# Performance work log

Hardware: AMD Instinct MI355X
Metric: run time of the kernel (lower is better)

Reference implementation:

```python
import jax, jax.numpy as jnp
import numpy as np

EPS = 1e-5
N_NODES = 100000
N_EDGES = 1600000
DIMS = [196, 64, 128, 256, 256, 576]


def sage_conv(x, src, dst, Wl, Wr, b, n):
    # PyG SAGEConv (mean aggr): out = lin_l(mean_j x_j) + lin_r(x_i)
    agg = jax.ops.segment_sum(x[src], dst, num_segments=n)
    cnt = jax.ops.segment_sum(jnp.ones((src.shape[0],), x.dtype), dst, num_segments=n)
    agg = agg / jnp.maximum(cnt, 1.0)[:, None]
    return agg @ Wl.T + x @ Wr.T + b


def batch_norm(x, gamma, beta):
    m = jnp.mean(x, axis=0)
    v = jnp.mean((x - m) ** 2, axis=0)  # biased var, as in torch BN forward
    return (x - m) * jax.lax.rsqrt(v + EPS) * gamma + beta


def setup_inputs() -> dict:
    key = jax.random.key(0)
    ks = jax.random.split(key, 32)
    inp = {
        "x": jax.random.normal(ks[0], (N_NODES, DIMS[0]), dtype=jnp.float32),
        "edge_index": jax.random.randint(ks[1], (2, N_EDGES), 0, N_NODES, dtype=jnp.int32),
    }
    ki = 2
    for i in range(5):
        fin, fout = DIMS[i], DIMS[i + 1]
        s = 1.0 / np.sqrt(fin)
        inp[f"W{i+1}l"] = jax.random.uniform(ks[ki], (fout, fin), jnp.float32, -s, s); ki += 1
        inp[f"W{i+1}r"] = jax.random.uniform(ks[ki], (fout, fin), jnp.float32, -s, s); ki += 1
        inp[f"b{i+1}"] = jax.random.uniform(ks[ki], (fout,), jnp.float32, -s, s); ki += 1
    for i in range(4):
        fout = DIMS[i + 1]
        inp[f"g{i+1}"] = jnp.ones((fout,), jnp.float32)
        inp[f"be{i+1}"] = jnp.zeros((fout,), jnp.float32)
    return inp


def reference(x, edge_index,
              W1l, W1r, b1, W2l, W2r, b2, W3l, W3r, b3,
              W4l, W4r, b4, W5l, W5r, b5,
              g1, be1, g2, be2, g3, be3, g4, be4):
    src, dst = edge_index[0], edge_index[1]
    n = x.shape[0]
    x = jax.nn.relu(batch_norm(sage_conv(x, src, dst, W1l, W1r, b1, n), g1, be1))
    x = jax.nn.relu(batch_norm(sage_conv(x, src, dst, W2l, W2r, b2, n), g2, be2))
    x = jax.nn.relu(batch_norm(sage_conv(x, src, dst, W3l, W3r, b3, n), g3, be3))
    x = jax.nn.relu(batch_norm(sage_conv(x, src, dst, W4l, W4r, b4, n), g4, be4))
    x = sage_conv(x, src, dst, W5l, W5r, b5, n)
    return x
```

## Files before the change

### kernel.cpp

```cpp
#include <hip/hip_runtime.h>
#include <hip/hip_bf16.h>

typedef __hip_bfloat16 bf16;
typedef __attribute__((ext_vector_type(8))) short short8;
typedef __attribute__((ext_vector_type(4))) float f32x4;

#define NN 100000
#define NE 1600000

__device__ __forceinline__ float bf2f(short s) {
    return __uint_as_float(((unsigned int)(unsigned short)s) << 16);
}
__device__ __forceinline__ short f2bf(float f) {
    union { bf16 b; short s; } u;
    u.b = __float2bfloat16(f);
    return u.s;
}

__global__ void detect_kernel(const unsigned int* __restrict__ x, int* __restrict__ flags) {
    __shared__ int s;
    if (threadIdx.x == 0) s = 0;
    __syncthreads();
    int c = 0;
    for (int j = 0; j < 4; ++j) {
        unsigned int w = x[threadIdx.x * 4 + j];
        unsigned int e = (w >> 7) & 0xFF;
        if (e >= 100 && e <= 141) c++;
    }
    atomicAdd(&s, c);
    __syncthreads();
    if (threadIdx.x == 0) flags[0] = (s > 128) ? 1 : 0;
}

__global__ __launch_bounds__(256) void cvt_pad_kernel(const void* __restrict__ in,
                                                      bf16* __restrict__ out,
                                                      int rows, int sk, int dk,
                                                      const int* __restrict__ flagp) {
    int i = blockIdx.x * 256 + threadIdx.x;
    int g4 = dk >> 2;
    if (i >= rows * g4) return;
    int row = i / g4;
    int c = (i - row * g4) * 4;
    uint2 w;
    w.x = 0u; w.y = 0u;
    if (c < sk) {
        if (flagp[0]) {
            w = *(const uint2*)((const char*)in + ((size_t)row * sk + c) * 2);
        } else {
            const float* f = (const float*)((const char*)in + ((size_t)row * sk + c) * 4);
            union { bf16 t[4]; uint2 u; } pk;
            pk.t[0] = __float2bfloat16(f[0]);
            pk.t[1] = __float2bfloat16(f[1]);
            pk.t[2] = __float2bfloat16(f[2]);
            pk.t[3] = __float2bfloat16(f[3]);
            w = pk.u;
        }
    }
    *(uint2*)((char*)out + ((size_t)row * dk + c) * 2) = w;
}

struct WJobs {
    const void* src[10];
    bf16* dst[10];
    int rows[10];
    int sk[10];
    int dk[10];
};
__global__ __launch_bounds__(256) void cvt_pad_multi(WJobs J, const int* __restrict__ flagp) {
    int j = blockIdx.y;
    int g4 = J.dk[j] >> 2;
    int tot = J.rows[j] * g4;
    int i = blockIdx.x * 256 + threadIdx.x;
    if (i >= tot) return;
    int row = i / g4;
    int c = (i - row * g4) * 4;
    int sk = J.sk[j];
    uint2 w;
    w.x = 0u; w.y = 0u;
    if (c < sk) {
        if (flagp[0]) {
            w = *(const uint2*)((const char*)J.src[j] + ((size_t)row * sk + c) * 2);
        } else {
            const float* f = (const float*)((const char*)J.src[j] + ((size_t)row * sk + c) * 4);
            union { bf16 t[4]; uint2 u; } pk;
            pk.t[0] = __float2bfloat16(f[0]);
            pk.t[1] = __float2bfloat16(f[1]);
            pk.t[2] = __float2bfloat16(f[2]);
            pk.t[3] = __float2bfloat16(f[3]);
            w = pk.u;
        }
    }
    *(uint2*)((char*)J.dst[j] + ((size_t)row * J.dk[j] + c) * 2) = w;
}

struct VJobs {
    const void* src[13];
    float* dst[13];
    int n[13];
};
__global__ __launch_bounds__(576) void cvt_f32_multi(VJobs J, const int* __restrict__ flagp) {
    int j = blockIdx.x;
    int c = threadIdx.x;
    if (c >= J.n[j]) return;
    float v;
    if (flagp[0]) v = __bfloat162float(((const bf16*)J.src[j])[c]);
    else v = ((const float*)J.src[j])[c];
    J.dst[j][c] = v;
}

__global__ __launch_bounds__(256) void fill_kernel(bf16* __restrict__ out, long long n) {
    long long i = (long long)blockIdx.x * 256 + threadIdx.x;
    if (i < n) out[i] = __float2bfloat16(1000.0f);
}


__global__ __launch_bounds__(256) void count_kernel(const int* __restrict__ dst,
                                                    int* __restrict__ cnt) {
    int e = blockIdx.x * 256 + threadIdx.x;
    if (e < NE) atomicAdd(&cnt[dst[e]], 1);
}

#define SCAN_NB ((NN + 1023) / 1024)

__global__ __launch_bounds__(256) void scan_partial_kernel(const int* __restrict__ cnt,
                                                           int* __restrict__ bsum) {
    __shared__ int lds[256];
    int t = threadIdx.x;
    int base = blockIdx.x * 1024 + t * 4;
    int s = 0;
#pragma unroll
    for (int i = 0; i < 4; ++i) {
        int idx = base + i;
        if (idx < NN) s += cnt[idx];
    }
    lds[t] = s;
    __syncthreads();
    for (int h = 128; h > 0; h >>= 1) {
        if (t < h) lds[t] += lds[t + h];
        __syncthreads();
    }
    if (t == 0) bsum[blockIdx.x] = lds[0];
}

__global__ __launch_bounds__(128) void scan_bsum_kernel(int* __restrict__ bsum,
                                                        int* __restrict__ indptr) {
    __shared__ int lds[128];
    int t = threadIdx.x;
    int v = (t < SCAN_NB) ? bsum[t] : 0;
    lds[t] = v;
    __syncthreads();
    for (int off = 1; off < 128; off <<= 1) {
        int x = (t >= off) ? lds[t - off] : 0;
        __syncthreads();
        lds[t] += x;
        __syncthreads();
    }
    if (t < SCAN_NB) bsum[t] = lds[t] - v;
    if (t == 127) indptr[NN] = lds[127];
}

__global__ __launch_bounds__(256) void scan_apply_kernel(const int* __restrict__ cnt,
                                                         const int* __restrict__ bsum,
                                                         int* __restrict__ indptr,
                                                         int* __restrict__ cursor,
                                                         float* __restrict__ recip) {
    __shared__ int lds[256];
    int t = threadIdx.x;
    int base = blockIdx.x * 1024 + t * 4;
    int c[4];
    int s = 0;
#pragma unroll
    for (int i = 0; i < 4; ++i) {
        int idx = base + i;
        c[i] = (idx < NN) ? cnt[idx] : 0;
        s += c[i];
    }
    lds[t] = s;
    __syncthreads();
    for (int off = 1; off < 256; off <<= 1) {
        int x = (t >= off) ? lds[t - off] : 0;
        __syncthreads();
        lds[t] += x;
        __syncthreads();
    }
    int run = bsum[blockIdx.x] + lds[t] - s;
#pragma unroll
    for (int i = 0; i < 4; ++i) {
        int idx = base + i;
        if (idx < NN) {
            indptr[idx] = run;
            cursor[idx] = run;
            recip[idx] = 1.0f / (float)(c[i] > 1 ? c[i] : 1);
            run += c[i];
        }
    }
}

__global__ __launch_bounds__(256) void scatter_kernel(const int* __restrict__ src,
                                                      const int* __restrict__ dst,
                                                      int* __restrict__ cursor,
                                                      int* __restrict__ csr) {
    int e = blockIdx.x * 256 + threadIdx.x;
    if (e < NE) {
        int d = dst[e];
        int p = atomicAdd(&cursor[d], 1);
        csr[p] = src[e];
    }
}

template <int D, int ADD>
__global__ __launch_bounds__(256) void aggv_kernel(const bf16* __restrict__ u,
                                                   const int* __restrict__ indptr,
                                                   const int* __restrict__ csr,
                                                   const float* __restrict__ recip,
                                                   bf16* __restrict__ out) {
    constexpr int TPR = D / 8;
    constexpr int NPB = 256 / TPR;
    const int tid = threadIdx.x;
    const int node = blockIdx.x * NPB + tid / TPR;
    if (node >= NN) return;
    const int c0 = (tid % TPR) * 8;
    const short* ub = (const short*)u + c0;
    const int j0 = indptr[node], j1 = indptr[node + 1];
    float acc[8];
#pragma unroll
    for (int t = 0; t < 8; ++t) acc[t] = 0.f;
    int j = j0;
    for (; j + 3 < j1; j += 4) {
        int s0 = csr[j], s1 = csr[j + 1], s2 = csr[j + 2], s3 = csr[j + 3];
        short8 v0 = *(const short8*)(ub + (size_t)s0 * D);
        short8 v1 = *(const short8*)(ub + (size_t)s1 * D);
        short8 v2 = *(const short8*)(ub + (size_t)s2 * D);
        short8 v3 = *(const short8*)(ub + (size_t)s3 * D);
#pragma unroll
        for (int t = 0; t < 8; ++t)
            acc[t] += (bf2f(v0[t]) + bf2f(v1[t])) + (bf2f(v2[t]) + bf2f(v3[t]));
    }
    for (; j < j1; ++j) {
        short8 v0 = *(const short8*)(ub + (size_t)csr[j] * D);
#pragma unroll
        for (int t = 0; t < 8; ++t) acc[t] += bf2f(v0[t]);
    }
    const float r = recip[node];
    size_t o = (size_t)node * D + c0;
    short8 w;
    if (ADD) {
        short8 prev = *(const short8*)((const short*)out + o);
#pragma unroll
        for (int t = 0; t < 8; ++t) w[t] = f2bf(acc[t] * r + bf2f(prev[t]));
    } else {
#pragma unroll
        for (int t = 0; t < 8; ++t) w[t] = f2bf(acc[t] * r);
    }
    *(short8*)((short*)out + o) = w;
}

template <int D>
__global__ __launch_bounds__(256) void aggbn_kernel(const bf16* __restrict__ raw,
                                                    const int* __restrict__ indptr,
                                                    const int* __restrict__ csr,
                                                    const float* __restrict__ recip,
                                                    const float* __restrict__ scale,
                                                    const float* __restrict__ shift,
                                                    bf16* __restrict__ act,
                                                    bf16* __restrict__ agg) {
    constexpr int TPR = D / 8;
    constexpr int NPB = 256 / TPR;
    const int tid = threadIdx.x;
    const int node = blockIdx.x * NPB + tid / TPR;
    if (node >= NN) return;
    const int c0 = (tid % TPR) * 8;
    float sc[8], sh[8];
    *(float4*)&sc[0] = *(const float4*)&scale[c0];
    *(float4*)&sc[4] = *(const float4*)&scale[c0 + 4];
    *(float4*)&sh[0] = *(const float4*)&shift[c0];
    *(float4*)&sh[4] = *(const float4*)&shift[c0 + 4];
    const short* ub = (const short*)raw + c0;
    {
        short8 v = *(const short8*)(ub + (size_t)node * D);
        short8 w;
#pragma unroll
        for (int t = 0; t < 8; ++t) {
            float x = bf2f(v[t]) * sc[t] + sh[t];
            w[t] = f2bf(x > 0.f ? x : 0.f);
        }
        *(short8*)((short*)act + (size_t)node * D + c0) = w;
    }
    const int j0 = indptr[node], j1 = indptr[node + 1];
    float acc[8];
#pragma unroll
    for (int t = 0; t < 8; ++t) acc[t] = 0.f;
    int j = j0;
    for (; j + 3 < j1; j += 4) {
        int s0 = csr[j], s1 = csr[j + 1], s2 = csr[j + 2], s3 = csr[j + 3];
        short8 v0 = *(const short8*)(ub + (size_t)s0 * D);
        short8 v1 = *(const short8*)(ub + (size_t)s1 * D);
        short8 v2 = *(const short8*)(ub + (size_t)s2 * D);
        short8 v3 = *(const short8*)(ub + (size_t)s3 * D);
#pragma unroll
        for (int t = 0; t < 8; ++t) {
            float x0 = fmaxf(bf2f(v0[t]) * sc[t] + sh[t], 0.f);
            float x1 = fmaxf(bf2f(v1[t]) * sc[t] + sh[t], 0.f);
            float x2 = fmaxf(bf2f(v2[t]) * sc[t] + sh[t], 0.f);
            float x3 = fmaxf(bf2f(v3[t]) * sc[t] + sh[t], 0.f);
            acc[t] += (x0 + x1) + (x2 + x3);
        }
    }
    for (; j < j1; ++j) {
        short8 v0 = *(const short8*)(ub + (size_t)csr[j] * D);
#pragma unroll
        for (int t = 0; t < 8; ++t)
            acc[t] += fmaxf(bf2f(v0[t]) * sc[t] + sh[t], 0.f);
    }
    const float r = recip[node];
    size_t o = (size_t)node * D + c0;
    short8 w;
#pragma unroll
    for (int t = 0; t < 8; ++t) w[t] = f2bf(acc[t] * r);
    *(short8*)((short*)agg + o) = w;
}

__device__ __forceinline__ void gld_lds16(const void* g, void* l) {
    __builtin_amdgcn_global_load_lds(
        (const __attribute__((address_space(1))) unsigned int*)g,
        (__attribute__((address_space(3))) unsigned int*)l, 16, 0, 0);
}

__global__ __launch_bounds__(256) void gemm_kernel(
    const bf16* __restrict__ A1, const bf16* __restrict__ W1, int K1,
    const bf16* __restrict__ A2, const bf16* __restrict__ W2, int K2,
    const float* __restrict__ bias,
    bf16* __restrict__ outB, bf16* __restrict__ outB2, int Nsplit,
    void* __restrict__ outFinal,
    float* __restrict__ statp,
    const int* __restrict__ flagp,
    int M, int N) {
    __shared__ alignas(16) char smem[81920];

    const int tid = threadIdx.x;
    const int lane = tid & 63, wv = tid >> 6;
    const int lrow = lane & 15, lq = lane >> 4;

    const int nwg = gridDim.x * gridDim.y;
    const int flat = blockIdx.y * gridDim.x + blockIdx.x;
    const int xcd = flat & 7;
    const int rest = flat >> 3;
    const int q = nwg >> 3, r = nwg & 7;
    const int chunk = (xcd < r) ? xcd * (q + 1) : r * (q + 1) + (xcd - r) * q;
    const int newid = chunk + rest;
    const int n0 = (newid % gridDim.x) * 64;
    const int m0 = (newid / gridDim.x) * 256;

    const int isbf = flagp[0];

    f32x4 acc[4][4];
#pragma unroll
    for (int a = 0; a < 4; ++a)
#pragma unroll
        for (int b = 0; b < 4; ++b) acc[a][b] = (f32x4){0.f, 0.f, 0.f, 0.f};

    const int sr = tid >> 3;
    const int scb = (tid & 7) << 4;

    const int nt1 = K1 >> 6;
    const int nt2 = K2 >> 6;
    const int nt = nt1 + nt2;

    auto stage = [&](int t, int b) {
        const bf16* Ap;
        const bf16* Wp;
        int K, k0;
        if (t < nt1) { Ap = A1; Wp = W1; K = K1; k0 = t << 6; }
        else { Ap = A2; Wp = W2; K = K2; k0 = (t - nt1) << 6; }
        char* bA = smem + b * 40960;
        char* bW = bA + 32768;
#pragma unroll
        for (int i = 0; i < 8; ++i) {
            int row = i * 32 + sr;
            int gr = m0 + row;
            if (gr >= M) gr = M - 1;
            const char* g = (const char*)Ap + ((size_t)gr * K + k0) * 2 +
                            (scb ^ ((row & 7) << 4));
            gld_lds16(g, bA + row * 128 + scb);
        }
#pragma unroll
        for (int i = 0; i < 2; ++i) {
            int row = i * 32 + sr;
            const char* g = (const char*)Wp + ((size_t)(n0 + row) * K + k0) * 2 +
                            (scb ^ ((row & 7) << 4));
            gld_lds16(g, bW + row * 128 + scb);
        }
    };

    stage(0, 0);
    __syncthreads();
    int cur = 0;
#pragma unroll 1
    for (int t = 0; t < nt; ++t) {
        if (t + 1 < nt) stage(t + 1, cur ^ 1);
        const char* sA = smem + cur * 40960;
        const char* sW = sA + 32768;
#pragma unroll
        for (int kh = 0; kh < 2; ++kh) {
            short8 a[4], b[4];
            const int cb = kh * 64 + lq * 16;
#pragma unroll
            for (int mi = 0; mi < 4; ++mi) {
                int row = wv * 64 + mi * 16 + lrow;
                a[mi] = *(const short8*)(sA + row * 128 + (cb ^ ((row & 7) << 4)));
            }
#pragma unroll
            for (int ni = 0; ni < 4; ++ni) {
                int row = ni * 16 + lrow;
                b[ni] = *(const short8*)(sW + row * 128 + (cb ^ ((row & 7) << 4)));
            }
#pragma unroll
            for (int mi = 0; mi < 4; ++mi)
#pragma unroll
                for (int ni = 0; ni < 4; ++ni)
                    acc[mi][ni] = __builtin_amdgcn_mfma_f32_16x16x32_bf16(
                        a[mi], b[ni], acc[mi][ni], 0, 0, 0);
        }
        __syncthreads();
        cur ^= 1;
    }

    if (statp) {
#pragma unroll
        for (int ni = 0; ni < 4; ++ni) {
            int gcol = n0 + ni * 16 + lrow;
            float bv = bias ? bias[gcol] : 0.f;
            float s = 0.f, q2 = 0.f;
#pragma unroll
            for (int mi = 0; mi < 4; ++mi) {
#pragma unroll
                for (int r2 = 0; r2 < 4; ++r2) {
                    int grow = m0 + wv * 64 + mi * 16 + lq * 4 + r2;
                    if (grow < M) {
                        float v = acc[mi][ni][r2] + bv;
                        s += v;
                        q2 += v * v;
                    }
                }
            }
            s += __shfl_xor(s, 16, 64);
            s += __shfl_xor(s, 32, 64);
            q2 += __shfl_xor(q2, 16, 64);
            q2 += __shfl_xor(q2, 32, 64);
            if (lq == 0) {
                atomicAdd(&statp[gcol], s);
                atomicAdd(&statp[N + gcol], q2);
            }
        }
    }
    const bool f32out = (outFinal != nullptr) && !isbf;
    if (!f32out) {
        bf16* dst = outB ? outB : (bf16*)outFinal;
        short* sc = (short*)smem;
#pragma unroll
        for (int ni = 0; ni < 4; ++ni) {
            float bv = bias ? bias[n0 + ni * 16 + lrow] : 0.f;
#pragma unroll
            for (int mi = 0; mi < 4; ++mi) {
                int rl = wv * 64 + mi * 16 + lq * 4;
#pragma unroll
                for (int r2 = 0; r2 < 4; ++r2)
                    sc[(rl + r2) * 64 + ni * 16 + lrow] = f2bf(acc[mi][ni][r2] + bv);
            }
        }
        __syncthreads();
#pragma unroll
        for (int i = 0; i < 8; ++i) {
            int f8 = tid + i * 256;
            int rowl = f8 >> 3;
            int col0 = (f8 & 7) * 8;
            int grow = m0 + rowl;
            int gcol = n0 + col0;
            if (grow < M) {
                short8 v = ((const short8*)smem)[f8];
                if (gcol < Nsplit)
                    *(short8*)((short*)dst + (size_t)grow * Nsplit + gcol) = v;
                else
                    *(short8*)((short*)outB2 + (size_t)grow * (N - Nsplit) +
                               (gcol - Nsplit)) = v;
            }
        }
    } else {
        float* dst = (float*)outFinal;
        float* sf = (float*)smem;
#pragma unroll
        for (int ni = 0; ni < 4; ++ni) {
            float bv = bias ? bias[n0 + ni * 16 + lrow] : 0.f;
#pragma unroll
            for (int mi = 0; mi < 4; ++mi) {
                int rl = wv * 64 + mi * 16 + lq * 4;
#pragma unroll
                for (int r2 = 0; r2 < 4; ++r2)
                    sf[(rl + r2) * 64 + ni * 16 + lrow] = acc[mi][ni][r2] + bv;
            }
        }
        __syncthreads();
#pragma unroll
        for (int i = 0; i < 16; ++i) {
            int f4 = tid + i * 256;
            int rowl = f4 >> 4;
            int col0 = (f4 & 15) * 4;
            int grow = m0 + rowl;
            if (grow < M)
                *(float4*)(dst + (size_t)grow * N + n0 + col0) =
                    ((const float4*)smem)[f4];
        }
    }
}


__global__ __launch_bounds__(256) void bn_stats_kernel(const bf16* __restrict__ C,
                                                       int ldN,
                                                       float* __restrict__ stats) {
    int N = 1 << ldN;
    int tid = threadIdx.x;
    int c = tid & (N - 1);
    int rsub = tid >> ldN;
    int rstep = 256 >> ldN;
    int r0 = blockIdx.x * 64;
    float s = 0.f, q = 0.f;
    for (int r = r0 + rsub; r < r0 + 64; r += rstep) {
        if (r < NN) {
            float v = __bfloat162float(C[(size_t)r * N + c]);
            s += v;
            q += v * v;
        }
    }
    __shared__ float ls[256], lq[256];
    ls[tid] = s;
    lq[tid] = q;
    __syncthreads();
    for (int half = rstep >> 1; half > 0; half >>= 1) {
        if (rsub < half) {
            ls[tid] += ls[tid + half * N];
            lq[tid] += lq[tid + half * N];
        }
        __syncthreads();
    }
    if (rsub == 0) {
        atomicAdd(&stats[c], ls[tid]);
        atomicAdd(&stats[N + c], lq[tid]);
    }
}

__global__ __launch_bounds__(256) void bn_finalize_kernel(const float* __restrict__ stats,
                                                          const float* __restrict__ g,
                                                          const float* __restrict__ be,
                                                          int N,
                                                          float* __restrict__ scale,
                                                          float* __restrict__ shift) {
    int c = threadIdx.x;
    if (c >= N) return;
    float mean = stats[c] * (1.0f / NN);
    float var = stats[N + c] * (1.0f / NN) - mean * mean;
    var = fmaxf(var, 0.f);
    float sc = g[c] * rsqrtf(var + 1e-5f);
    scale[c] = sc;
    shift[c] = be[c] - mean * sc;
}


extern "C" void kernel_launch(void* const* d_in, const int* in_sizes, int n_in,
                              void* d_out, int out_size, void* d_ws, size_t ws_size,
                              hipStream_t stream) {
    const void* x_raw = d_in[0];
    const int* ei = (const int*)d_in[1];
    const int* src = ei;
    const int* dst = ei + NE;

    char* w = (char*)d_ws;
    size_t off = 0;
    auto alloc = [&](size_t bytes) {
        void* p = w + off;
        off = (off + bytes + 255) & ~(size_t)255;
        return p;
    };
    int* flags = (int*)alloc(256);
    int* cnt = (int*)alloc((size_t)NN * 4);
    int* indptr = (int*)alloc((size_t)(NN + 1) * 4);
    int* cursor = (int*)alloc((size_t)NN * 4);
    float* recip = (float*)alloc((size_t)NN * 4);
    int* csr = (int*)alloc((size_t)NE * 4);
    int* bsum = (int*)alloc((size_t)SCAN_NB * 4);
    const int KDIM[5] = {196, 64, 128, 256, 256};
    const int KPAD[5] = {256, 64, 128, 256, 256};
    const int NDIM[5] = {64, 128, 256, 256, 576};
    bf16 *Wlb[5], *Wrb[5];
    float *bf_[5], *gf[4], *bef[4];
    for (int i = 0; i < 5; ++i) {
        Wlb[i] = (bf16*)alloc((size_t)KPAD[i] * NDIM[i] * 2);
        Wrb[i] = (bf16*)alloc((size_t)KPAD[i] * NDIM[i] * 2);
        bf_[i] = (float*)alloc((size_t)NDIM[i] * 4);
    }
    for (int i = 0; i < 4; ++i) {
        gf[i] = (float*)alloc((size_t)NDIM[i] * 4);
        bef[i] = (float*)alloc((size_t)NDIM[i] * 4);
    }
    float* bias1cat = (float*)alloc(128 * 4);
    float* stats = (float*)alloc(1408 * 4);
    float* scale = (float*)alloc(256 * 4);
    float* shift = (float*)alloc(256 * 4);
    float *s1 = stats, *s2 = stats + 128, *s3 = stats + 384, *s4 = stats + 896;
    bf16* aggb = (bf16*)alloc((size_t)NN * 256 * 2);
    bf16* S1 = (bf16*)alloc((size_t)NN * 256 * 2);
    bf16* S2 = (bf16*)alloc((size_t)NN * 256 * 2);
    bf16* xb = aggb;
    bf16* u1 = S2;

    if (off > ws_size) {
        long long n = (long long)NN * 576;
        fill_kernel<<<(int)((n + 255) / 256), 256, 0, stream>>>((bf16*)d_out, n);
        return;
    }

    hipMemsetAsync(cnt, 0, (size_t)NN * 4, stream);
    hipMemsetAsync(stats, 0, 1408 * 4, stream);
    hipMemsetAsync(bias1cat, 0, 64 * 4, stream);

    detect_kernel<<<1, 64, 0, stream>>>((const unsigned int*)x_raw, flags);

    {
        int totx = NN * (KPAD[0] >> 2);
        cvt_pad_kernel<<<(totx + 255) / 256, 256, 0, stream>>>(x_raw, xb, NN, 196, 256, flags);

        WJobs wj;
        int maxb = 0;
        for (int i = 0; i < 5; ++i) {
            wj.src[2 * i] = d_in[2 + 3 * i];
            wj.dst[2 * i] = Wlb[i];
            wj.src[2 * i + 1] = d_in[3 + 3 * i];
            wj.dst[2 * i + 1] = Wrb[i];
            wj.rows[2 * i] = wj.rows[2 * i + 1] = NDIM[i];
            wj.sk[2 * i] = wj.sk[2 * i + 1] = KDIM[i];
            wj.dk[2 * i] = wj.dk[2 * i + 1] = KPAD[i];
            int nb = (NDIM[i] * (KPAD[i] >> 2) + 255) / 256;
            if (nb > maxb) maxb = nb;
        }
        cvt_pad_multi<<<dim3(maxb, 10), 256, 0, stream>>>(wj, flags);

        VJobs vj;
        vj.src[0] = d_in[4];  vj.dst[0] = bias1cat + 64; vj.n[0] = 64;
        for (int i = 1; i < 5; ++i) {
            vj.src[i] = d_in[4 + 3 * i];
            vj.dst[i] = bf_[i];
            vj.n[i] = NDIM[i];
        }
        for (int i = 0; i < 4; ++i) {
            vj.src[5 + i] = d_in[17 + 2 * i];
            vj.dst[5 + i] = gf[i];
            vj.n[5 + i] = NDIM[i];
            vj.src[9 + i] = d_in[18 + 2 * i];
            vj.dst[9 + i] = bef[i];
            vj.n[9 + i] = NDIM[i];
        }
        cvt_f32_multi<<<13, 576, 0, stream>>>(vj, flags);
    }

    count_kernel<<<(NE + 255) / 256, 256, 0, stream>>>(dst, cnt);
    scan_partial_kernel<<<SCAN_NB, 256, 0, stream>>>(cnt, bsum);
    scan_bsum_kernel<<<1, 128, 0, stream>>>(bsum, indptr);
    scan_apply_kernel<<<SCAN_NB, 256, 0, stream>>>(cnt, bsum, indptr, cursor, recip);
    scatter_kernel<<<(NE + 255) / 256, 256, 0, stream>>>(src, dst, cursor, csr);

    const int GM = (NN + 63) / 64;
    const int GY = (NN + 255) / 256;

    gemm_kernel<<<dim3(2, GY), 256, 0, stream>>>(xb, Wlb[0], 256, nullptr, nullptr, 0,
                                                 bias1cat, u1, S1, 64,
                                                 nullptr, nullptr, flags, NN, 128);
    aggv_kernel<64, 1><<<NN / 32, 256, 0, stream>>>(u1, indptr, csr, recip, S1);
    bn_stats_kernel<<<GM, 256, 0, stream>>>(S1, 6, s1);
    bn_finalize_kernel<<<1, 256, 0, stream>>>(s1, gf[0], bef[0], 64, scale, shift);

    aggbn_kernel<64><<<NN / 32, 256, 0, stream>>>(S1, indptr, csr, recip, scale, shift,
                                                  S2, aggb);
    gemm_kernel<<<dim3(2, GY), 256, 0, stream>>>(aggb, Wlb[1], 64, S2, Wrb[1], 64,
                                                 bf_[1], S1, nullptr, 128,
                                                 nullptr, s2, flags, NN, 128);
    bn_finalize_kernel<<<1, 256, 0, stream>>>(s2, gf[1], bef[1], 128, scale, shift);

    aggbn_kernel<128><<<NN / 16, 256, 0, stream>>>(S1, indptr, csr, recip, scale, shift,
                                                   S2, aggb);
    gemm_kernel<<<dim3(4, GY), 256, 0, stream>>>(aggb, Wlb[2], 128, S2, Wrb[2], 128,
                                                 bf_[2], S1, nullptr, 256,
                                                 nullptr, s3, flags, NN, 256);
    bn_finalize_kernel<<<1, 256, 0, stream>>>(s3, gf[2], bef[2], 256, scale, shift);

    aggbn_kernel<256><<<NN / 8, 256, 0, stream>>>(S1, indptr, csr, recip, scale, shift,
                                                  S2, aggb);
    gemm_kernel<<<dim3(4, GY), 256, 0, stream>>>(aggb, Wlb[3], 256, S2, Wrb[3], 256,
                                                 bf_[3], S1, nullptr, 256,
                                                 nullptr, s4, flags, NN, 256);
    bn_finalize_kernel<<<1, 256, 0, stream>>>(s4, gf[3], bef[3], 256, scale, shift);

    aggbn_kernel<256><<<NN / 8, 256, 0, stream>>>(S1, indptr, csr, recip, scale, shift,
                                                  S2, aggb);
    gemm_kernel<<<dim3(9, GY), 256, 0, stream>>>(aggb, Wlb[4], 256, S2, Wrb[4], 256,
                                                 bf_[4], nullptr, nullptr, 576,
                                                 d_out, nullptr, flags, NN, 576);
}
```

Before: 1.249 ms.

## Single-buffer GEMM LDS to raise occupancy and unroll gather loops by eight

The GEMM kernel drops its double-buffered LDS staging (80 KB) for a single 40 KB buffer with sync before and after each load. This lets more workgroups fit per CU, at the cost of losing the overlap between loading one tile and computing the previous one. The fp32 epilogue is split into two halves so it fits in the smaller buffer. Separately, both aggregation kernels gain an 8-way unrolled neighbor-gather loop so more independent row loads are in flight at once.

After: 1.271 ms. About the same (+1.7%).

```diff
diff --git a/kernel.cpp b/kernel.cpp
--- a/kernel.cpp
+++ b/kernel.cpp
@@ -226,6 +226,18 @@
 #pragma unroll
     for (int t = 0; t < 8; ++t) acc[t] = 0.f;
     int j = j0;
+    for (; j + 7 < j1; j += 8) {
+        int s[8];
+#pragma unroll
+        for (int u8 = 0; u8 < 8; ++u8) s[u8] = csr[j + u8];
+        short8 v[8];
+#pragma unroll
+        for (int u8 = 0; u8 < 8; ++u8) v[u8] = *(const short8*)(ub + (size_t)s[u8] * D);
+#pragma unroll
+        for (int t = 0; t < 8; ++t)
+            acc[t] += ((bf2f(v[0][t]) + bf2f(v[1][t])) + (bf2f(v[2][t]) + bf2f(v[3][t]))) +
+                      ((bf2f(v[4][t]) + bf2f(v[5][t])) + (bf2f(v[6][t]) + bf2f(v[7][t])));
+    }
     for (; j + 3 < j1; j += 4) {
         int s0 = csr[j], s1 = csr[j + 1], s2 = csr[j + 2], s3 = csr[j + 3];
         short8 v0 = *(const short8*)(ub + (size_t)s0 * D);
@@ -291,6 +303,26 @@
 #pragma unroll
     for (int t = 0; t < 8; ++t) acc[t] = 0.f;
     int j = j0;
+    for (; j + 7 < j1; j += 8) {
+        int s[8];
+#pragma unroll
+        for (int u8 = 0; u8 < 8; ++u8) s[u8] = csr[j + u8];
+        short8 v[8];
+#pragma unroll
+        for (int u8 = 0; u8 < 8; ++u8) v[u8] = *(const short8*)(ub + (size_t)s[u8] * D);
+#pragma unroll
+        for (int t = 0; t < 8; ++t) {
+            float a0 = fmaxf(bf2f(v[0][t]) * sc[t] + sh[t], 0.f) +
+                       fmaxf(bf2f(v[1][t]) * sc[t] + sh[t], 0.f);
+            float a1 = fmaxf(bf2f(v[2][t]) * sc[t] + sh[t], 0.f) +
+                       fmaxf(bf2f(v[3][t]) * sc[t] + sh[t], 0.f);
+            float a2 = fmaxf(bf2f(v[4][t]) * sc[t] + sh[t], 0.f) +
+                       fmaxf(bf2f(v[5][t]) * sc[t] + sh[t], 0.f);
+            float a3 = fmaxf(bf2f(v[6][t]) * sc[t] + sh[t], 0.f) +
+                       fmaxf(bf2f(v[7][t]) * sc[t] + sh[t], 0.f);
+            acc[t] += (a0 + a1) + (a2 + a3);
+        }
+    }
     for (; j + 3 < j1; j += 4) {
         int s0 = csr[j], s1 = csr[j + 1], s2 = csr[j + 2], s3 = csr[j + 3];
         short8 v0 = *(const short8*)(ub + (size_t)s0 * D);
@@ -335,7 +367,9 @@
     float* __restrict__ statp,
     const int* __restrict__ flagp,
     int M, int N) {
-    __shared__ alignas(16) char smem[81920];
+    __shared__ alignas(16) char smem[40960];
+    char* sA = smem;
+    char* sW = smem + 32768;
 
     const int tid = threadIdx.x;
     const int lane = tid & 63, wv = tid >> 6;
@@ -362,67 +396,54 @@
     const int sr = tid >> 3;
     const int scb = (tid & 7) << 4;
 
-    const int nt1 = K1 >> 6;
-    const int nt2 = K2 >> 6;
-    const int nt = nt1 + nt2;
-
-    auto stage = [&](int t, int b) {
-        const bf16* Ap;
-        const bf16* Wp;
-        int K, k0;
-        if (t < nt1) { Ap = A1; Wp = W1; K = K1; k0 = t << 6; }
-        else { Ap = A2; Wp = W2; K = K2; k0 = (t - nt1) << 6; }
-        char* bA = smem + b * 40960;
-        char* bW = bA + 32768;
-#pragma unroll
-        for (int i = 0; i < 8; ++i) {
-            int row = i * 32 + sr;
-            int gr = m0 + row;
-            if (gr >= M) gr = M - 1;
-            const char* g = (const char*)Ap + ((size_t)gr * K + k0) * 2 +
-                            (scb ^ ((row & 7) << 4));
-            gld_lds16(g, bA + row * 128 + scb);
-        }
-#pragma unroll
-        for (int i = 0; i < 2; ++i) {
-            int row = i * 32 + sr;
-            const char* g = (const char*)Wp + ((size_t)(n0 + row) * K + k0) * 2 +
-                            (scb ^ ((row & 7) << 4));
-            gld_lds16(g, bW + row * 128 + scb);
-        }
-    };
-
-    stage(0, 0);
-    __syncthreads();
-    int cur = 0;
 #pragma unroll 1
-    for (int t = 0; t < nt; ++t) {
-        if (t + 1 < nt) stage(t + 1, cur ^ 1);
-        const char* sA = smem + cur * 40960;
-        const char* sW = sA + 32768;
-#pragma unroll
-        for (int kh = 0; kh < 2; ++kh) {
-            short8 a[4], b[4];
-            const int cb = kh * 64 + lq * 16;
-#pragma unroll
-            for (int mi = 0; mi < 4; ++mi) {
-                int row = wv * 64 + mi * 16 + lrow;
-                a[mi] = *(const short8*)(sA + row * 128 + (cb ^ ((row & 7) << 4)));
-            }
-#pragma unroll
-            for (int ni = 0; ni < 4; ++ni) {
-                int row = ni * 16 + lrow;
-                b[ni] = *(const short8*)(sW + row * 128 + (cb ^ ((row & 7) << 4)));
-            }
-#pragma unroll
-            for (int mi = 0; mi < 4; ++mi)
-#pragma unroll
-                for (int ni = 0; ni < 4; ++ni)
-                    acc[mi][ni] = __builtin_amdgcn_mfma_f32_16x16x32_bf16(
-                        a[mi], b[ni], acc[mi][ni], 0, 0, 0);
-        }
-        __syncthreads();
-        cur ^= 1;
+    for (int seg = 0; seg < 2; ++seg) {
+        const bf16* Ap = seg ? A2 : A1;
+        const bf16* Wp = seg ? W2 : W1;
+        const int K = seg ? K2 : K1;
+        if (K == 0) continue;
+#pragma unroll 1
+        for (int k0 = 0; k0 < K; k0 += 64) {
+            __syncthreads();
+#pragma unroll
+            for (int i = 0; i < 8; ++i) {
+                int row = i * 32 + sr;
+                int gr = m0 + row;
+                if (gr >= M) gr = M - 1;
+                const char* g = (const char*)Ap + ((size_t)gr * K + k0) * 2 +
+                                (scb ^ ((row & 7) << 4));
+                gld_lds16(g, sA + row * 128 + scb);
+            }
+#pragma unroll
+            for (int i = 0; i < 2; ++i) {
+                int row = i * 32 + sr;
+                const char* g = (const char*)Wp + ((size_t)(n0 + row) * K + k0) * 2 +
+                                (scb ^ ((row & 7) << 4));
+                gld_lds16(g, sW + row * 128 + scb);
+            }
+            __syncthreads();
+#pragma unroll
+            for (int kh = 0; kh < 2; ++kh) {
+                short8 a[4], b[4];
+                const int cb = kh * 64 + lq * 16;
+#pragma unroll
+                for (int mi = 0; mi < 4; ++mi) {
+                    int row = wv * 64 + mi * 16 + lrow;
+                    a[mi] = *(const short8*)(sA + row * 128 + (cb ^ ((row & 7) << 4)));
+                }
+#pragma unroll
+                for (int ni = 0; ni < 4; ++ni) {
+                    int row = ni * 16 + lrow;
+                    b[ni] = *(const short8*)(sW + row * 128 + (cb ^ ((row & 7) << 4)));
+                }
+#pragma unroll
+                for (int mi = 0; mi < 4; ++mi)
+#pragma unroll
+                    for (int ni = 0; ni < 4; ++ni)
+                        acc[mi][ni] = __builtin_amdgcn_mfma_f32_16x16x32_bf16(
+                            a[mi], b[ni], acc[mi][ni], 0, 0, 0);
+            }
+        }
     }
 
     if (statp) {
@@ -453,6 +474,7 @@
             }
         }
     }
+    __syncthreads();
     const bool f32out = (outFinal != nullptr) && !isbf;
     if (!f32out) {
         bf16* dst = outB ? outB : (bf16*)outFinal;
@@ -488,27 +510,33 @@
     } else {
         float* dst = (float*)outFinal;
         float* sf = (float*)smem;
-#pragma unroll
-        for (int ni = 0; ni < 4; ++ni) {
-            float bv = bias ? bias[n0 + ni * 16 + lrow] : 0.f;
-#pragma unroll
-            for (int mi = 0; mi < 4; ++mi) {
-                int rl = wv * 64 + mi * 16 + lq * 4;
-#pragma unroll
-                for (int r2 = 0; r2 < 4; ++r2)
-                    sf[(rl + r2) * 64 + ni * 16 + lrow] = acc[mi][ni][r2] + bv;
-            }
-        }
-        __syncthreads();
-#pragma unroll
-        for (int i = 0; i < 16; ++i) {
-            int f4 = tid + i * 256;
-            int rowl = f4 >> 4;
-            int col0 = (f4 & 15) * 4;
-            int grow = m0 + rowl;
-            if (grow < M)
-                *(float4*)(dst + (size_t)grow * N + n0 + col0) =
-                    ((const float4*)smem)[f4];
+#pragma unroll 1
+        for (int h = 0; h < 2; ++h) {
+            if ((wv >> 1) == h) {
+#pragma unroll
+                for (int ni = 0; ni < 4; ++ni) {
+                    float bv = bias ? bias[n0 + ni * 16 + lrow] : 0.f;
+#pragma unroll
+                    for (int mi = 0; mi < 4; ++mi) {
+                        int rl = (wv & 1) * 64 + mi * 16 + lq * 4;
+#pragma unroll
+                        for (int r2 = 0; r2 < 4; ++r2)
+                            sf[(rl + r2) * 64 + ni * 16 + lrow] = acc[mi][ni][r2] + bv;
+                    }
+                }
+            }
+            __syncthreads();
+#pragma unroll
+            for (int i = 0; i < 8; ++i) {
+                int f4 = tid + i * 256;
+                int rowl = f4 >> 4;
+                int col0 = (f4 & 15) * 4;
+                int grow = m0 + h * 128 + rowl;
+                if (grow < M)
+                    *(float4*)(dst + (size_t)grow * N + n0 + col0) =
+                        ((const float4*)smem)[f4];
+            }
+            __syncthreads();
         }
     }
 }
```
